# Kernel optimization log

Measured on AMD Instinct MI355X. Metric: run time of the kernel, lower is better.

Reference implementation:

```python
import jax, jax.numpy as jnp
import numpy as np

B, C, H, W = 8, 96, 256, 256
KH, KW = 7, 7


def setup_inputs() -> dict:
    key = jax.random.key(0)
    k1, k2, k3 = jax.random.split(key, 3)
    x = jax.random.normal(k1, (B, C, H, W), dtype=jnp.float32)
    # kaiming_normal fan_out, relu: std = sqrt(2 / fan_out); fan_out = C*k for these shapes
    std_h = float(np.sqrt(2.0 / (C * KH)))
    std_w = float(np.sqrt(2.0 / (C * KW)))
    weight_h = jax.random.normal(k2, (C, 1, KH, 1), dtype=jnp.float32) * std_h
    weight_w = jax.random.normal(k3, (C, 1, 1, KW), dtype=jnp.float32) * std_w
    r = jnp.asarray(1.5, dtype=jnp.float32)  # fractional radius exercises bilinear path
    return {"x": x, "weight_h": weight_h, "weight_w": weight_w, "r": r}


def _axial(x, taps, r, axis):
    """Continuous-offset depthwise conv along one axis.

    x: [B,C,H,W]; taps: [k, C] per-tap depthwise weights; axis: 2 (h) or 3 (w).
    Equivalent to looped grid_sample(align_corners=True, padding_mode='zeros')
    with normalized shift offset*r*2/(size-1), i.e. a pixel shift of offset*r.
    """
    size = x.shape[axis]
    k = taps.shape[0]
    pad = k // 2
    coords = jnp.arange(size, dtype=x.dtype)
    out = jnp.zeros_like(x)
    shp = [1, 1, 1, 1]
    shp[axis] = size
    for i, off in enumerate(range(-pad, pad + 1)):
        pos = coords + off * r                     # sampling position in pixels
        i0f = jnp.floor(pos)
        frac = (pos - i0f).reshape(shp)
        i0 = i0f.astype(jnp.int32)
        i1 = i0 + 1
        m0 = ((i0 >= 0) & (i0 < size)).astype(x.dtype).reshape(shp)
        m1 = ((i1 >= 0) & (i1 < size)).astype(x.dtype).reshape(shp)
        g0 = jnp.take(x, jnp.clip(i0, 0, size - 1), axis=axis) * m0
        g1 = jnp.take(x, jnp.clip(i1, 0, size - 1), axis=axis) * m1
        samp = g0 * (1.0 - frac) + g1 * frac       # bilinear along shifted axis
        out = out + samp * taps[i][None, :, None, None]
    return out


def reference(x, weight_h, weight_w, r):
    # clamp(r, min=1.0) with torch grad semantics (grad 1 at r == 1.0)
    r_val = jnp.where(r < 1.0, jnp.asarray(1.0, x.dtype), r)
    taps_h = weight_h[:, 0, :, 0].T  # [KH, C]
    taps_w = weight_w[:, 0, 0, :].T  # [KW, C]
    return x + _axial(x, taps_h, r_val, 2) + _axial(x, taps_w, r_val, 3)
```

## Files before the change

kernel.cpp:

```cpp
#include <hip/hip_runtime.h>


constexpr int B = 8, C = 96, H = 256, W = 256;
constexpr int KT = 7;
constexpr int HALO = 8;
constexpr int NW = 2 * HALO + 1;
constexpr int RPW = 4;
constexpr int RPB = 16;


__global__ __launch_bounds__(64) void build_stencils(
    const float* __restrict__ wh,
    const float* __restrict__ ww,
    const float* __restrict__ rp,
    float* __restrict__ ws)
{
    const int c = blockIdx.x;
    const int d = threadIdx.x;
    if (d >= NW) return;

    float r = rp[0];
    if (r < 1.0f) r = 1.0f;

    float av = 0.f, aw = 0.f;
#pragma unroll
    for (int i = 0; i < KT; ++i) {
        float s   = (float)(i - 3) * r;
        float d0f = floorf(s);
        int   d0  = (int)d0f;
        float f   = s - d0f;
        float thv = wh[c * KT + i];
        float twv = ww[c * KT + i];
        if (d - HALO == d0)     { av = fmaf(thv, 1.f - f, av); aw = fmaf(twv, 1.f - f, aw); }
        if (d - HALO == d0 + 1) { av = fmaf(thv, f, av);       aw = fmaf(twv, f, aw); }
    }
    ws[c * NW + d]          = av;
    ws[C * NW + c * NW + d] = aw;
}

__global__ __launch_bounds__(256) void axialdw_kernel(
    const float* __restrict__ x,
    const float* __restrict__ ws,
    float* __restrict__ out)
{
    constexpr int NWG = B * C * (H / RPB);
    constexpr int CPX = NWG / 8;
    const int bid = blockIdx.x;
    const int lb  = (bid & 7) * CPX + (bid >> 3);

    const int hb   = lb % (H / RPB);
    const int bc   = lb / (H / RPB);
    const int c    = bc % C;
    const int wave = threadIdx.x >> 6;
    const int lane = threadIdx.x & 63;
    const int r0   = hb * RPB + wave * RPW;
    const int w0   = lane * 4;

    float wtv[NW], wth[NW];
#pragma unroll
    for (int d = 0; d < NW; ++d) {
        wtv[d] = ws[c * NW + d];
        wth[d] = ws[C * NW + c * NW + d];
    }

    const float* plane = x + (size_t)bc * (H * W);

    float nbv[16][4];
#pragma unroll
    for (int i = 0; i < 16; ++i) {
        const int j  = (i < 8) ? (i - 8) : (i - 4);
        const int hh = r0 + j;
        bool need = false;
#pragma unroll
        for (int rr = 0; rr < RPW; ++rr) {
            const int d = j - rr + HALO;
            if (d >= 0 && d < NW) need = need || (wtv[d] != 0.f);
        }
        float4 v = make_float4(0.f, 0.f, 0.f, 0.f);
        if (need && hh >= 0 && hh < H)
            v = *(const float4*)(plane + (size_t)hh * W + w0);
        nbv[i][0] = v.x; nbv[i][1] = v.y; nbv[i][2] = v.z; nbv[i][3] = v.w;
    }

    float acc[RPW][4];
    float ctr[RPW][4];
#pragma unroll
    for (int rr = 0; rr < RPW; ++rr) {
        const float* row = plane + (size_t)(r0 + rr) * W;

        float sp[20];
#pragma unroll
        for (int k = 0; k < 5; ++k) {
            const int wb = w0 - 8 + 4 * k;
            float4 v;
            if (k == 2) {
                v = *(const float4*)(row + wb);
            } else {
                const bool ok = ((unsigned)wb < (unsigned)W);
                v = *(const float4*)(row + (ok ? wb : 0));
                const float m = ok ? 1.f : 0.f;
                v.x *= m; v.y *= m; v.z *= m; v.w *= m;
            }
            sp[4 * k + 0] = v.x; sp[4 * k + 1] = v.y;
            sp[4 * k + 2] = v.z; sp[4 * k + 3] = v.w;
        }

#pragma unroll
        for (int e = 0; e < 4; ++e) {
            ctr[rr][e] = sp[HALO + e];
            acc[rr][e] = sp[HALO + e];
        }
#pragma unroll
        for (int d = 0; d < NW; ++d) {
            const float wg = wth[d];
#pragma unroll
            for (int e = 0; e < 4; ++e)
                acc[rr][e] = fmaf(wg, sp[d + e], acc[rr][e]);
        }
    }

#pragma unroll
    for (int rr = 0; rr < RPW; ++rr) {
#pragma unroll
        for (int d = 0; d < NW; ++d) {
            const float wg = wtv[d];
            const int j = rr + d - HALO;
#pragma unroll
            for (int e = 0; e < 4; ++e) {
                float s;
                if (j >= 0 && j <= 3)      s = ctr[j][e];
                else if (j < 0)            s = nbv[j + 8][e];
                else                       s = nbv[j + 4][e];
                acc[rr][e] = fmaf(wg, s, acc[rr][e]);
            }
        }
    }

    float* obase = out + (size_t)bc * (H * W);
#pragma unroll
    for (int rr = 0; rr < RPW; ++rr) {
        float4 o;
        o.x = acc[rr][0]; o.y = acc[rr][1]; o.z = acc[rr][2]; o.w = acc[rr][3];
        *(float4*)(obase + (size_t)(r0 + rr) * W + w0) = o;
    }
}

extern "C" void kernel_launch(void* const* d_in, const int* in_sizes, int n_in,
                              void* d_out, int out_size, void* d_ws, size_t ws_size,
                              hipStream_t stream) {
    const float* x  = (const float*)d_in[0];
    const float* wh = (const float*)d_in[1];
    const float* ww = (const float*)d_in[2];
    const float* rp = (const float*)d_in[3];
    float* out = (float*)d_out;
    float* ws  = (float*)d_ws;

    build_stencils<<<C, 64, 0, stream>>>(wh, ww, rp, ws);
    const int blocks = B * C * (H / RPB);
    axialdw_kernel<<<blocks, 256, 0, stream>>>(x, ws, out);
}
```

Measured before the change: 361.6 us.

## Stage row tile with halo in LDS via global_load_lds and reuse across waves

Each block now copies its 16 output rows plus 8-row vertical halos into a padded shared-memory tile using direct global-to-LDS loads, with zeroed column padding. Both the horizontal and vertical stencils then read from LDS, replacing redundant per-wave global loads of neighbor rows and masked edge loads. Multiply-adds for zero horizontal weights are skipped, and launch bounds request 4 blocks per CU. In exchange the kernel uses about 34KB of LDS per block and adds a block-wide barrier.

```diff
diff --git a/kernel.cpp b/kernel.cpp
--- a/kernel.cpp
+++ b/kernel.cpp
@@ -5,8 +5,9 @@
 constexpr int KT = 7;
 constexpr int HALO = 8;
 constexpr int NW = 2 * HALO + 1;
-constexpr int RPW = 4;
 constexpr int RPB = 16;
+constexpr int SR = RPB + 2 * HALO;
+constexpr int LDW = W + 16;
 
 
 __global__ __launch_bounds__(64) void build_stencils(
@@ -38,11 +39,13 @@
     ws[C * NW + c * NW + d] = aw;
 }
 
-__global__ __launch_bounds__(256) void axialdw_kernel(
+__global__ __launch_bounds__(256, 4) void axialdw_kernel(
     const float* __restrict__ x,
     const float* __restrict__ ws,
     float* __restrict__ out)
 {
+    __shared__ float tile[SR][LDW];
+
     constexpr int NWG = B * C * (H / RPB);
     constexpr int CPX = NWG / 8;
     const int bid = blockIdx.x;
@@ -51,10 +54,35 @@
     const int hb   = lb % (H / RPB);
     const int bc   = lb / (H / RPB);
     const int c    = bc % C;
-    const int wave = threadIdx.x >> 6;
-    const int lane = threadIdx.x & 63;
-    const int r0   = hb * RPB + wave * RPW;
+    const int tid  = threadIdx.x;
+    const int wave = tid >> 6;
+    const int lane = tid & 63;
     const int w0   = lane * 4;
+
+    const float* plane = x + (size_t)bc * (H * W);
+    const int gr0 = hb * RPB - HALO;
+
+#pragma unroll
+    for (int it = 0; it < SR / 4; ++it) {
+        const int i  = wave + 4 * it;
+        const int gr = gr0 + i;
+        if (gr >= 0 && gr < H) {
+            const float* gsrc = plane + (size_t)gr * W + w0;
+            __builtin_amdgcn_global_load_lds(
+                (const __attribute__((address_space(1))) void*)gsrc,
+                (__attribute__((address_space(3))) void*)&tile[i][HALO],
+                16, 0, 0);
+        } else {
+            *(float4*)&tile[i][HALO + w0] = make_float4(0.f, 0.f, 0.f, 0.f);
+        }
+    }
+
+    if (tid < SR * 4) {
+        const int i = tid >> 2;
+        const int q = tid & 3;
+        const int col = (q < 2) ? q * 4 : (W + (q - 2) * 4 + 8);
+        *(float4*)&tile[i][col] = make_float4(0.f, 0.f, 0.f, 0.f);
+    }
 
     float wtv[NW], wth[NW];
 #pragma unroll
@@ -63,48 +91,22 @@
         wth[d] = ws[C * NW + c * NW + d];
     }
 
-    const float* plane = x + (size_t)bc * (H * W);
+    __syncthreads();
 
-    float nbv[16][4];
+    const int rbase = wave * 4;
+
+    float acc[4][4];
+    float ctr[4][4];
 #pragma unroll
-    for (int i = 0; i < 16; ++i) {
-        const int j  = (i < 8) ? (i - 8) : (i - 4);
-        const int hh = r0 + j;
-        bool need = false;
-#pragma unroll
-        for (int rr = 0; rr < RPW; ++rr) {
-            const int d = j - rr + HALO;
-            if (d >= 0 && d < NW) need = need || (wtv[d] != 0.f);
-        }
-        float4 v = make_float4(0.f, 0.f, 0.f, 0.f);
-        if (need && hh >= 0 && hh < H)
-            v = *(const float4*)(plane + (size_t)hh * W + w0);
-        nbv[i][0] = v.x; nbv[i][1] = v.y; nbv[i][2] = v.z; nbv[i][3] = v.w;
-    }
-
-    float acc[RPW][4];
-    float ctr[RPW][4];
-#pragma unroll
-    for (int rr = 0; rr < RPW; ++rr) {
-        const float* row = plane + (size_t)(r0 + rr) * W;
-
+    for (int rr = 0; rr < 4; ++rr) {
+        const float* lrow = &tile[rbase + 8 + rr][w0];
         float sp[20];
 #pragma unroll
         for (int k = 0; k < 5; ++k) {
-            const int wb = w0 - 8 + 4 * k;
-            float4 v;
-            if (k == 2) {
-                v = *(const float4*)(row + wb);
-            } else {
-                const bool ok = ((unsigned)wb < (unsigned)W);
-                v = *(const float4*)(row + (ok ? wb : 0));
-                const float m = ok ? 1.f : 0.f;
-                v.x *= m; v.y *= m; v.z *= m; v.w *= m;
-            }
+            const float4 v = *(const float4*)(lrow + 4 * k);
             sp[4 * k + 0] = v.x; sp[4 * k + 1] = v.y;
             sp[4 * k + 2] = v.z; sp[4 * k + 3] = v.w;
         }
-
 #pragma unroll
         for (int e = 0; e < 4; ++e) {
             ctr[rr][e] = sp[HALO + e];
@@ -113,35 +115,50 @@
 #pragma unroll
         for (int d = 0; d < NW; ++d) {
             const float wg = wth[d];
+            if (wg != 0.f) {
 #pragma unroll
-            for (int e = 0; e < 4; ++e)
-                acc[rr][e] = fmaf(wg, sp[d + e], acc[rr][e]);
+                for (int e = 0; e < 4; ++e)
+                    acc[rr][e] = fmaf(wg, sp[d + e], acc[rr][e]);
+            }
         }
     }
 
 #pragma unroll
-    for (int rr = 0; rr < RPW; ++rr) {
+    for (int s = 0; s < 20; ++s) {
+        float v[4];
+        if (s >= 8 && s <= 11) {
 #pragma unroll
-        for (int d = 0; d < NW; ++d) {
-            const float wg = wtv[d];
-            const int j = rr + d - HALO;
+            for (int e = 0; e < 4; ++e) v[e] = ctr[s - 8][e];
+        } else {
+            bool need = false;
 #pragma unroll
-            for (int e = 0; e < 4; ++e) {
-                float s;
-                if (j >= 0 && j <= 3)      s = ctr[j][e];
-                else if (j < 0)            s = nbv[j + 8][e];
-                else                       s = nbv[j + 4][e];
-                acc[rr][e] = fmaf(wg, s, acc[rr][e]);
+            for (int rr = 0; rr < 4; ++rr) {
+                const int d = s - rr;
+                if (d >= 0 && d < NW) need = need || (wtv[d] != 0.f);
+            }
+            if (!need) continue;
+            const float4 t = *(const float4*)&tile[rbase + s][HALO + w0];
+            v[0] = t.x; v[1] = t.y; v[2] = t.z; v[3] = t.w;
+        }
+#pragma unroll
+        for (int rr = 0; rr < 4; ++rr) {
+            const int d = s - rr;
+            if (d >= 0 && d < NW) {
+                const float wg = wtv[d];
+#pragma unroll
+                for (int e = 0; e < 4; ++e)
+                    acc[rr][e] = fmaf(wg, v[e], acc[rr][e]);
             }
         }
     }
 
-    float* obase = out + (size_t)bc * (H * W);
+    float* obase = out + (size_t)bc * (H * W)
+                 + (size_t)(hb * RPB + rbase) * W + w0;
 #pragma unroll
-    for (int rr = 0; rr < RPW; ++rr) {
+    for (int rr = 0; rr < 4; ++rr) {
         float4 o;
         o.x = acc[rr][0]; o.y = acc[rr][1]; o.z = acc[rr][2]; o.w = acc[rr][3];
-        *(float4*)(obase + (size_t)(r0 + rr) * W + w0) = o;
+        *(float4*)(obase + (size_t)rr * W) = o;
     }
 }
 
```

Measured after the change: 339.5 us. -6.1%, faster.

## Shrink per-wave row tile and stream vertical taps to cut registers

Applied to the files above, without the earlier changes.

Each wave now computes 2 rows instead of 4, and the block covers 8 rows. Vertical neighbour rows are loaded one at a time and accumulated directly into both output rows, so the wave no longer holds a 16-row neighbour buffer. Zero-weight taps are skipped at runtime in both directions, launch bounds request higher occupancy, and outputs use nontemporal stores. In exchange, the redundant halo reads of vertical neighbours per output row roughly double, and the zero checks add divergence-free branches.

```diff
diff --git a/kernel.cpp b/kernel.cpp
--- a/kernel.cpp
+++ b/kernel.cpp
@@ -5,8 +5,12 @@
 constexpr int KT = 7;
 constexpr int HALO = 8;
 constexpr int NW = 2 * HALO + 1;
-constexpr int RPW = 4;
-constexpr int RPB = 16;
+constexpr int RPT = 2;
+constexpr int RPB = 8;
+constexpr int TILES = B * C * (H / RPB);
+constexpr int TPX = TILES / 8;
+
+typedef float f32x4 __attribute__((ext_vector_type(4)));
 
 
 __global__ __launch_bounds__(64) void build_stencils(
@@ -38,23 +42,21 @@
     ws[C * NW + c * NW + d] = aw;
 }
 
-__global__ __launch_bounds__(256) void axialdw_kernel(
+__global__ __launch_bounds__(256, 8) void axialdw_kernel(
     const float* __restrict__ x,
     const float* __restrict__ ws,
     float* __restrict__ out)
 {
-    constexpr int NWG = B * C * (H / RPB);
-    constexpr int CPX = NWG / 8;
     const int bid = blockIdx.x;
-    const int lb  = (bid & 7) * CPX + (bid >> 3);
+    const int lb  = (bid & 7) * TPX + (bid >> 3);
 
-    const int hb   = lb % (H / RPB);
-    const int bc   = lb / (H / RPB);
+    const int hb   = lb & (H / RPB - 1);
+    const int bc   = lb >> 5;
     const int c    = bc % C;
     const int wave = threadIdx.x >> 6;
     const int lane = threadIdx.x & 63;
-    const int r0   = hb * RPB + wave * RPW;
     const int w0   = lane * 4;
+    const int h0   = hb * RPB + wave * RPT;
 
     float wtv[NW], wth[NW];
 #pragma unroll
@@ -65,28 +67,38 @@
 
     const float* plane = x + (size_t)bc * (H * W);
 
-    float nbv[16][4];
+    float acc[RPT][4];
 #pragma unroll
-    for (int i = 0; i < 16; ++i) {
-        const int j  = (i < 8) ? (i - 8) : (i - 4);
-        const int hh = r0 + j;
-        bool need = false;
+    for (int rr = 0; rr < RPT; ++rr)
 #pragma unroll
-        for (int rr = 0; rr < RPW; ++rr) {
-            const int d = j - rr + HALO;
-            if (d >= 0 && d < NW) need = need || (wtv[d] != 0.f);
+        for (int e = 0; e < 4; ++e) acc[rr][e] = 0.f;
+
+#pragma unroll
+    for (int t = 0; t < NW + RPT - 1; ++t) {
+        const float g0 = (t < NW) ? wtv[t] : 0.f;
+        const float g1 = (t >= 1) ? wtv[t - 1] : 0.f;
+        if (g0 == 0.f && g1 == 0.f) continue;
+        const int hh = h0 + t - HALO;
+        if (hh < 0 || hh >= H) continue;
+        const float4 v = *(const float4*)(plane + (size_t)hh * W + w0);
+        if (g0 != 0.f) {
+            acc[0][0] = fmaf(g0, v.x, acc[0][0]);
+            acc[0][1] = fmaf(g0, v.y, acc[0][1]);
+            acc[0][2] = fmaf(g0, v.z, acc[0][2]);
+            acc[0][3] = fmaf(g0, v.w, acc[0][3]);
         }
-        float4 v = make_float4(0.f, 0.f, 0.f, 0.f);
-        if (need && hh >= 0 && hh < H)
-            v = *(const float4*)(plane + (size_t)hh * W + w0);
-        nbv[i][0] = v.x; nbv[i][1] = v.y; nbv[i][2] = v.z; nbv[i][3] = v.w;
+        if (g1 != 0.f) {
+            acc[1][0] = fmaf(g1, v.x, acc[1][0]);
+            acc[1][1] = fmaf(g1, v.y, acc[1][1]);
+            acc[1][2] = fmaf(g1, v.z, acc[1][2]);
+            acc[1][3] = fmaf(g1, v.w, acc[1][3]);
+        }
     }
 
-    float acc[RPW][4];
-    float ctr[RPW][4];
+    float* obase = out + (size_t)bc * (H * W) + (size_t)h0 * W + w0;
 #pragma unroll
-    for (int rr = 0; rr < RPW; ++rr) {
-        const float* row = plane + (size_t)(r0 + rr) * W;
+    for (int rr = 0; rr < RPT; ++rr) {
+        const float* row = plane + (size_t)(h0 + rr) * W;
 
         float sp[20];
 #pragma unroll
@@ -96,7 +108,7 @@
             if (k == 2) {
                 v = *(const float4*)(row + wb);
             } else {
-                const bool ok = ((unsigned)wb < (unsigned)W);
+                const bool ok = ((unsigned)wb <= (unsigned)(W - 4));
                 v = *(const float4*)(row + (ok ? wb : 0));
                 const float m = ok ? 1.f : 0.f;
                 v.x *= m; v.y *= m; v.z *= m; v.w *= m;
@@ -106,42 +118,21 @@
         }
 
 #pragma unroll
-        for (int e = 0; e < 4; ++e) {
-            ctr[rr][e] = sp[HALO + e];
-            acc[rr][e] = sp[HALO + e];
-        }
+        for (int e = 0; e < 4; ++e)
+            acc[rr][e] += sp[HALO + e];
 #pragma unroll
         for (int d = 0; d < NW; ++d) {
             const float wg = wth[d];
+            if (wg != 0.f) {
 #pragma unroll
-            for (int e = 0; e < 4; ++e)
-                acc[rr][e] = fmaf(wg, sp[d + e], acc[rr][e]);
-        }
-    }
-
-#pragma unroll
-    for (int rr = 0; rr < RPW; ++rr) {
-#pragma unroll
-        for (int d = 0; d < NW; ++d) {
-            const float wg = wtv[d];
-            const int j = rr + d - HALO;
-#pragma unroll
-            for (int e = 0; e < 4; ++e) {
-                float s;
-                if (j >= 0 && j <= 3)      s = ctr[j][e];
-                else if (j < 0)            s = nbv[j + 8][e];
-                else                       s = nbv[j + 4][e];
-                acc[rr][e] = fmaf(wg, s, acc[rr][e]);
+                for (int e = 0; e < 4; ++e)
+                    acc[rr][e] = fmaf(wg, sp[d + e], acc[rr][e]);
             }
         }
-    }
 
-    float* obase = out + (size_t)bc * (H * W);
-#pragma unroll
-    for (int rr = 0; rr < RPW; ++rr) {
-        float4 o;
+        f32x4 o;
         o.x = acc[rr][0]; o.y = acc[rr][1]; o.z = acc[rr][2]; o.w = acc[rr][3];
-        *(float4*)(obase + (size_t)(r0 + rr) * W + w0) = o;
+        __builtin_nontemporal_store(o, (f32x4*)(obase + (size_t)rr * W));
     }
 }
 
@@ -156,6 +147,5 @@
     float* ws  = (float*)d_ws;
 
     build_stencils<<<C, 64, 0, stream>>>(wh, ww, rp, ws);
-    const int blocks = B * C * (H / RPB);
-    axialdw_kernel<<<blocks, 256, 0, stream>>>(x, ws, out);
+    axialdw_kernel<<<TILES, 256, 0, stream>>>(x, ws, out);
 }
```

Result: slower. 419.7 us (+16.1%).
